# Kernel tuning notes

Measured on AMD Instinct MI355X. Metric: run time of the kernel, lower is better.

Reference implementation:

```python
import jax, jax.numpy as jnp
import numpy as np

NUM_LYR = 4
HIDDEN = 64
IN_DIM = 3
EMBED = 64  # embed_dim // pnt_cond_steps


def setup_inputs() -> dict:
    key = jax.random.key(0)
    ks = jax.random.split(key, 10)
    s = 0.05
    return {
        "x": jax.random.normal(ks[0], (256, 1, 4096, IN_DIM), dtype=jnp.float32),
        "proj_in_w": jax.random.normal(ks[1], (HIDDEN, IN_DIM), dtype=jnp.float32) * s,
        "proj_in_b": jax.random.normal(ks[2], (HIDDEN,), dtype=jnp.float32) * s,
        "lyr_w": jax.random.normal(ks[3], (NUM_LYR, HIDDEN, HIDDEN), dtype=jnp.float32) * s,
        "lyr_b": jax.random.normal(ks[4], (NUM_LYR, HIDDEN), dtype=jnp.float32) * s,
        "glyr_w": jax.random.normal(ks[5], (NUM_LYR, HIDDEN, 2 * HIDDEN), dtype=jnp.float32) * s,
        "glyr_b": jax.random.normal(ks[6], (NUM_LYR, HIDDEN), dtype=jnp.float32) * s,
        "proj_out_w": jax.random.normal(ks[7], (EMBED, HIDDEN * NUM_LYR), dtype=jnp.float32) * s,
        "proj_out_b": jax.random.normal(ks[8], (EMBED,), dtype=jnp.float32) * s,
    }


def reference(x, proj_in_w, proj_in_b, lyr_w, lyr_b, glyr_w, glyr_b, proj_out_w, proj_out_b):
    b, t, l, d = x.shape  # t == pnt_cond_steps, l == num_point (no resampling)
    h = x.reshape(b * t, l, d)
    # proj_in + ReLU: [B, L, hidden]
    h = jax.nn.relu(jnp.einsum('bld,hd->blh', h, proj_in_w) + proj_in_b)
    xs = []
    for i in range(NUM_LYR):
        h = jax.nn.relu(jnp.einsum('blh,oh->blo', h, lyr_w[i]) + lyr_b[i])
        g = jnp.max(h, axis=1, keepdims=True)  # global max-pool over points
        gx = jnp.concatenate([h, jnp.broadcast_to(g, h.shape)], axis=2)  # [B, L, 2*hidden]
        h = jax.nn.relu(jnp.einsum('blc,oc->blo', gx, glyr_w[i]) + glyr_b[i])
        xs.append(h)
    feat = jnp.concatenate(xs, axis=2)  # [B, L, hidden*num_lyr]
    out = jnp.einsum('blc,ec->ble', feat, proj_out_w) + proj_out_b
    out = jnp.max(out, axis=1)  # [B, embed]
    # rearrange '(b t) d -> b (d t)'
    out = out.reshape(b, t, -1)
    out = jnp.transpose(out, (0, 2, 1)).reshape(b, -1)
    return out
```

## Files before the change

### kernel.cpp

```cpp
#include <hip/hip_runtime.h>

#define HH   64
#define BPTS 256
#define LPB  4096
#define NBAT 256
#define NPTS (NBAT * LPB)

typedef _Float16 f16x8 __attribute__((ext_vector_type(8)));
typedef float    f32x4 __attribute__((ext_vector_type(4)));

__device__ __forceinline__ int fofs(int r, int c) {
    return (r << 6) | ((((c >> 3) ^ (r & 7))) << 3) | (c & 7);
}
__device__ __forceinline__ int bofs(int r, int m) {
    return (r << 6) | ((m ^ (r & 7)) << 3);
}
__device__ __forceinline__ f16x8 rd8(const _Float16* p, int r, int m) {
    return *(const f16x8*)&p[bofs(r, m)];
}

__device__ __forceinline__ void split2(float v, _Float16& h, _Float16& l) {
    h = (_Float16)v;
    l = (_Float16)(v - (float)h);
}

__device__ __forceinline__ void mfma_gemm(const _Float16* ah_, const _Float16* al_,
                                          const _Float16* wh_, const _Float16* wl_,
                                          int rb, int lane, f32x4 acc[2][4]) {
    const int rA = rb + (lane & 15);
    const int cB = lane & 15;
    const int g  = lane >> 4;
#pragma unroll
    for (int s = 0; s < 2; ++s) {
        const int m = s * 4 + g;
        f16x8 Ah[2], Al[2];
#pragma unroll
        for (int rt = 0; rt < 2; ++rt) {
            Ah[rt] = rd8(ah_, rA + 16 * rt, m);
            Al[rt] = rd8(al_, rA + 16 * rt, m);
        }
#pragma unroll
        for (int ct = 0; ct < 4; ++ct) {
            f16x8 Bh = rd8(wh_, cB + 16 * ct, m);
            f16x8 Bl = rd8(wl_, cB + 16 * ct, m);
#pragma unroll
            for (int rt = 0; rt < 2; ++rt) {
                acc[rt][ct] = __builtin_amdgcn_mfma_f32_16x16x32_f16(Ah[rt], Bh, acc[rt][ct], 0, 0, 0);
                acc[rt][ct] = __builtin_amdgcn_mfma_f32_16x16x32_f16(Ah[rt], Bl, acc[rt][ct], 0, 0, 0);
                acc[rt][ct] = __builtin_amdgcn_mfma_f32_16x16x32_f16(Al[rt], Bh, acc[rt][ct], 0, 0, 0);
            }
        }
    }
}

__device__ __forceinline__ void write_acts(_Float16* hi, _Float16* lo,
                                           const f32x4 t[2][4], int rb, int lane) {
    const int g = lane >> 4, cb = lane & 15;
#pragma unroll
    for (int rt = 0; rt < 2; ++rt)
#pragma unroll
        for (int reg = 0; reg < 4; ++reg) {
            const int r = rb + 16 * rt + 4 * g + reg;
#pragma unroll
            for (int ct = 0; ct < 4; ++ct) {
                _Float16 h, l;
                split2(t[rt][ct][reg], h, l);
                const int o = fofs(r, 16 * ct + cb);
                hi[o] = h; lo[o] = l;
            }
        }
}

__device__ __forceinline__ void stage_w(_Float16* wh, _Float16* wl,
                                        const float* __restrict__ W, int tid, int ldw) {
    const int o = tid >> 3, k0 = (tid & 7) << 3;
    const float* wr = &W[(size_t)o * ldw + k0];
    float4 a = *(const float4*)wr;
    float4 b = *(const float4*)(wr + 4);
    float v[8] = {a.x, a.y, a.z, a.w, b.x, b.y, b.z, b.w};
    f16x8 h, l;
#pragma unroll
    for (int i = 0; i < 8; ++i) { _Float16 hh, ll; split2(v[i], hh, ll); h[i] = hh; l[i] = ll; }
    const int ofs = bofs(o, k0 >> 3);
    *(f16x8*)&wh[ofs] = h;
    *(f16x8*)&wl[ofs] = l;
}

__device__ __forceinline__ unsigned encf(float f) {
    unsigned u = __float_as_uint(f);
    return (u & 0x80000000u) ? ~u : (u | 0x80000000u);
}
__device__ __forceinline__ float decf(unsigned u) {
    return (u & 0x80000000u) ? __uint_as_float(u ^ 0x80000000u) : __uint_as_float(~u);
}

__global__ __launch_bounds__(256) void k_init(float* gbuf, unsigned* oenc) {
    int i = blockIdx.x * 256 + threadIdx.x;
    if (i < 4 * NBAT * HH) gbuf[i] = 0.0f;
    if (i < NBAT * HH)     oenc[i] = 0x007FFFFFu;
}

__global__ __launch_bounds__(64) void k_goff(const float* __restrict__ g,
                                             const float* __restrict__ gw,
                                             const float* __restrict__ gb,
                                             float* __restrict__ goff, int li) {
    const int b = blockIdx.x, o = threadIdx.x;
    const float* gr = &g[b * HH];
    const float* wr = &gw[(size_t)li * 64 * 128 + o * 128 + 64];
    float s = gb[li * 64 + o];
#pragma unroll
    for (int k = 0; k < 64; k += 4) {
        float4 w4 = *(const float4*)&wr[k];
        float4 g4 = *(const float4*)&gr[k];
        s = fmaf(g4.x, w4.x, fmaf(g4.y, w4.y, fmaf(g4.z, w4.z, fmaf(g4.w, w4.w, s))));
    }
    goff[(size_t)b * HH + o] = s;
}

template<int NSTAGE, bool DO_OUT>
__global__ __launch_bounds__(512, 4) void k_fused(
    const float* __restrict__ x, const float* __restrict__ piw,
    const float* __restrict__ pib, const float* __restrict__ lyrw,
    const float* __restrict__ lyrb, const float* __restrict__ gw,
    const float* __restrict__ pw, const float* __restrict__ pob,
    const float* __restrict__ goffb, float* __restrict__ gmax,
    unsigned* __restrict__ oenc) {
    __shared__ __align__(16) _Float16 a_hi[BPTS * HH];
    __shared__ __align__(16) _Float16 a_lo[BPTS * HH];
    __shared__ __align__(16) _Float16 w_hi[HH * HH];
    __shared__ __align__(16) _Float16 w_lo[HH * HH];
    const int tid  = threadIdx.x;
    const int lane = tid & 63, wave = tid >> 6;
    const int rb   = wave << 5;
    const int pbase = blockIdx.x * BPTS;
    const int b = pbase / LPB;
    int ch4[4];
#pragma unroll
    for (int ct = 0; ct < 4; ++ct) ch4[ct] = 16 * ct + (lane & 15);

    stage_w(w_hi, w_lo, lyrw, tid, 64);
    {
        const int p = tid >> 1, half = tid & 1;
        const size_t pidx = (size_t)(pbase + p) * 3;
        const float x0 = x[pidx], x1 = x[pidx + 1], x2 = x[pidx + 2];
#pragma unroll
        for (int j = 0; j < 4; ++j) {
            const int o0 = half * 32 + j * 8;
            f16x8 h, l;
#pragma unroll
            for (int i = 0; i < 8; ++i) {
                const int o = o0 + i;
                float v = fmaxf(fmaf(piw[o * 3], x0,
                              fmaf(piw[o * 3 + 1], x1,
                              fmaf(piw[o * 3 + 2], x2, pib[o]))), 0.0f);
                _Float16 hh, ll; split2(v, hh, ll);
                h[i] = hh; l[i] = ll;
            }
            const int ofs = bofs(p, o0 >> 3);
            *(f16x8*)&a_hi[ofs] = h;
            *(f16x8*)&a_lo[ofs] = l;
        }
    }
    __syncthreads();

    f32x4 acc[2][4];
#pragma unroll
    for (int rt = 0; rt < 2; ++rt)
#pragma unroll
        for (int ct = 0; ct < 4; ++ct) {
            const float bb = lyrb[ch4[ct]];
            acc[rt][ct] = (f32x4){bb, bb, bb, bb};
        }
    mfma_gemm(a_hi, a_lo, w_hi, w_lo, rb, lane, acc);

    f32x4 oacc[2][4];
    if (DO_OUT) {
#pragma unroll
        for (int rt = 0; rt < 2; ++rt)
#pragma unroll
            for (int ct = 0; ct < 4; ++ct) oacc[rt][ct] = (f32x4){0.f, 0.f, 0.f, 0.f};
    }

    constexpr int NITER = DO_OUT ? 4 : (NSTAGE - 1);
#pragma unroll
    for (int li = 0; li < NITER; ++li) {
#pragma unroll
        for (int rt = 0; rt < 2; ++rt)
#pragma unroll
            for (int ct = 0; ct < 4; ++ct)
#pragma unroll
                for (int r = 0; r < 4; ++r)
                    acc[rt][ct][r] = fmaxf(acc[rt][ct][r], 0.0f);

        __syncthreads();
        write_acts(a_hi, a_lo, acc, rb, lane);
        stage_w(w_hi, w_lo, &gw[(size_t)li * 64 * 128], tid, 128);
        __syncthreads();

        f32x4 a2[2][4];
#pragma unroll
        for (int rt = 0; rt < 2; ++rt)
#pragma unroll
            for (int ct = 0; ct < 4; ++ct) {
                const float gv = goffb[(size_t)li * NBAT * HH + (size_t)b * HH + ch4[ct]];
                a2[rt][ct] = (f32x4){gv, gv, gv, gv};
            }
        mfma_gemm(a_hi, a_lo, w_hi, w_lo, rb, lane, a2);
#pragma unroll
        for (int rt = 0; rt < 2; ++rt)
#pragma unroll
            for (int ct = 0; ct < 4; ++ct)
#pragma unroll
                for (int r = 0; r < 4; ++r)
                    a2[rt][ct][r] = fmaxf(a2[rt][ct][r], 0.0f);

        __syncthreads();
        write_acts(a_hi, a_lo, a2, rb, lane);
        if (DO_OUT) {
            stage_w(w_hi, w_lo, &pw[(size_t)li * 64], tid, 256);
            __syncthreads();
            mfma_gemm(a_hi, a_lo, w_hi, w_lo, rb, lane, oacc);
            if (li < 3) {
                __syncthreads();
                stage_w(w_hi, w_lo, &lyrw[(size_t)(li + 1) * 4096], tid, 64);
                __syncthreads();
            }
        } else {
            stage_w(w_hi, w_lo, &lyrw[(size_t)(li + 1) * 4096], tid, 64);
            __syncthreads();
        }
        if (li < 3) {
#pragma unroll
            for (int rt = 0; rt < 2; ++rt)
#pragma unroll
                for (int ct = 0; ct < 4; ++ct) {
                    const float bb = lyrb[(li + 1) * 64 + ch4[ct]];
                    acc[rt][ct] = (f32x4){bb, bb, bb, bb};
                }
            mfma_gemm(a_hi, a_lo, w_hi, w_lo, rb, lane, acc);
        }
    }

    float m4[4];
    if (!DO_OUT) {
#pragma unroll
        for (int ct = 0; ct < 4; ++ct) m4[ct] = 0.0f;
#pragma unroll
        for (int rt = 0; rt < 2; ++rt)
#pragma unroll
            for (int ct = 0; ct < 4; ++ct)
#pragma unroll
                for (int r = 0; r < 4; ++r)
                    m4[ct] = fmaxf(m4[ct], fmaxf(acc[rt][ct][r], 0.0f));
    } else {
#pragma unroll
        for (int ct = 0; ct < 4; ++ct) m4[ct] = -3.4e38f;
#pragma unroll
        for (int rt = 0; rt < 2; ++rt)
#pragma unroll
            for (int ct = 0; ct < 4; ++ct)
#pragma unroll
                for (int r = 0; r < 4; ++r)
                    m4[ct] = fmaxf(m4[ct], oacc[rt][ct][r]);
    }
#pragma unroll
    for (int ct = 0; ct < 4; ++ct) {
        m4[ct] = fmaxf(m4[ct], __shfl_xor(m4[ct], 16, 64));
        m4[ct] = fmaxf(m4[ct], __shfl_xor(m4[ct], 32, 64));
    }
    __syncthreads();
    float* red = (float*)a_hi;
    if ((lane >> 4) == 0)
#pragma unroll
        for (int ct = 0; ct < 4; ++ct)
            red[wave * 64 + ct * 16 + (lane & 15)] = m4[ct];
    __syncthreads();
    if (tid < 64) {
        float v = red[tid];
#pragma unroll
        for (int w = 1; w < 8; ++w) v = fmaxf(v, red[w * 64 + tid]);
        if (!DO_OUT)
            atomicMax((unsigned*)&gmax[b * HH + tid], __float_as_uint(v));
        else
            atomicMax(&oenc[b * HH + tid], encf(v + pob[tid]));
    }
}

__global__ __launch_bounds__(256) void k_dec(const unsigned* __restrict__ oenc,
                                             float* __restrict__ out) {
    int i = blockIdx.x * 256 + threadIdx.x;
    out[i] = decf(oenc[i]);
}

extern "C" void kernel_launch(void* const* d_in, const int* in_sizes, int n_in,
                              void* d_out, int out_size, void* d_ws, size_t ws_size,
                              hipStream_t stream) {
    const float* x    = (const float*)d_in[0];
    const float* piw  = (const float*)d_in[1];
    const float* pib  = (const float*)d_in[2];
    const float* lyrw = (const float*)d_in[3];
    const float* lyrb = (const float*)d_in[4];
    const float* gw   = (const float*)d_in[5];
    const float* gb   = (const float*)d_in[6];
    const float* pw   = (const float*)d_in[7];
    const float* pob  = (const float*)d_in[8];
    float* out = (float*)d_out;

    float* gbuf    = (float*)d_ws;
    unsigned* oenc = (unsigned*)(gbuf + 4 * NBAT * HH);
    float* goffbuf = (float*)(oenc + NBAT * HH);

    const int nblk = NPTS / BPTS;

    k_init<<<256, 256, 0, stream>>>(gbuf, oenc);

    k_fused<1, false><<<nblk, 512, 0, stream>>>(x, piw, pib, lyrw, lyrb, gw, pw, pob,
                                                goffbuf, gbuf, oenc);
    k_goff<<<NBAT, 64, 0, stream>>>(gbuf, gw, gb, goffbuf, 0);

    k_fused<2, false><<<nblk, 512, 0, stream>>>(x, piw, pib, lyrw, lyrb, gw, pw, pob,
                                                goffbuf, gbuf + NBAT * HH, oenc);
    k_goff<<<NBAT, 64, 0, stream>>>(gbuf + NBAT * HH, gw, gb, goffbuf + NBAT * HH, 1);

    k_fused<3, false><<<nblk, 512, 0, stream>>>(x, piw, pib, lyrw, lyrb, gw, pw, pob,
                                                goffbuf, gbuf + 2 * NBAT * HH, oenc);
    k_goff<<<NBAT, 64, 0, stream>>>(gbuf + 2 * NBAT * HH, gw, gb, goffbuf + 2 * NBAT * HH, 2);

    k_fused<4, false><<<nblk, 512, 0, stream>>>(x, piw, pib, lyrw, lyrb, gw, pw, pob,
                                                goffbuf, gbuf + 3 * NBAT * HH, oenc);
    k_goff<<<NBAT, 64, 0, stream>>>(gbuf + 3 * NBAT * HH, gw, gb, goffbuf + 3 * NBAT * HH, 3);

    k_fused<4, true><<<nblk, 512, 0, stream>>>(x, piw, pib, lyrw, lyrb, gw, pw, pob,
                                               goffbuf, nullptr, oenc);

    k_dec<<<(NBAT * HH) / 256, 256, 0, stream>>>(oenc, out);
}
```

Measured before the change: 1.058 ms.

## Materialize intermediate activations in workspace instead of recomputing prefix layers

The old code re-ran every earlier layer from the raw input in each of five passes, so the total compute grew quadratically with depth. The new code stores each layer's activations in global workspace as packed hi/lo fp16 pairs. It also keeps a running fp32 partial sum of the output projection, so each pass runs only one new layer. The small global-offset kernel is folded into the main kernels, each computing the offset per lane. This trades recomputation for large global memory traffic (about 268MB per activation buffer), and it depends on the workspace being large enough, with fallbacks for smaller sizes.

```diff
diff --git a/kernel.cpp b/kernel.cpp
--- a/kernel.cpp
+++ b/kernel.cpp
@@ -9,11 +9,13 @@
 typedef _Float16 f16x8 __attribute__((ext_vector_type(8)));
 typedef float    f32x4 __attribute__((ext_vector_type(4)));
 
+union HL { unsigned u; _Float16 f[2]; };
+
+__device__ __forceinline__ int bofs(int r, int m) {
+    return (r << 6) | ((m ^ (r & 7)) << 3);
+}
 __device__ __forceinline__ int fofs(int r, int c) {
     return (r << 6) | ((((c >> 3) ^ (r & 7))) << 3) | (c & 7);
-}
-__device__ __forceinline__ int bofs(int r, int m) {
-    return (r << 6) | ((m ^ (r & 7)) << 3);
 }
 __device__ __forceinline__ f16x8 rd8(const _Float16* p, int r, int m) {
     return *(const f16x8*)&p[bofs(r, m)];
@@ -22,6 +24,9 @@
 __device__ __forceinline__ void split2(float v, _Float16& h, _Float16& l) {
     h = (_Float16)v;
     l = (_Float16)(v - (float)h);
+}
+__device__ __forceinline__ unsigned pack_hilo(float v) {
+    HL u; split2(v, u.f[0], u.f[1]); return u.u;
 }
 
 __device__ __forceinline__ void mfma_gemm(const _Float16* ah_, const _Float16* al_,
@@ -86,6 +91,41 @@
     *(f16x8*)&wl[ofs] = l;
 }
 
+__device__ __forceinline__ void stage_u(_Float16* hi, _Float16* lo,
+                                        const unsigned* __restrict__ u,
+                                        int pbase, int tid) {
+    const int row = tid >> 1, c0 = (tid & 1) << 5;
+    const unsigned* src = &u[(size_t)(pbase + row) * HH + c0];
+#pragma unroll
+    for (int j = 0; j < 4; ++j) {
+        uint4 qa = *(const uint4*)&src[j * 8];
+        uint4 qb = *(const uint4*)&src[j * 8 + 4];
+        unsigned q[8] = {qa.x, qa.y, qa.z, qa.w, qb.x, qb.y, qb.z, qb.w};
+        f16x8 h, l;
+#pragma unroll
+        for (int i = 0; i < 8; ++i) { HL v; v.u = q[i]; h[i] = v.f[0]; l[i] = v.f[1]; }
+        const int ofs = bofs(row, (c0 >> 3) + j);
+        *(f16x8*)&hi[ofs] = h;
+        *(f16x8*)&lo[ofs] = l;
+    }
+}
+
+__device__ __forceinline__ float goff_lane_calc(const float* __restrict__ gall,
+                                                const float* __restrict__ gw,
+                                                const float* __restrict__ gb,
+                                                int li, int b, int lane) {
+    const float* gr = &gall[((size_t)li * NBAT + b) * HH];
+    const float* wr = &gw[((size_t)li * 64 + lane) * 128 + 64];
+    float s = gb[li * 64 + lane];
+#pragma unroll
+    for (int k = 0; k < 64; k += 4) {
+        float4 w4 = *(const float4*)&wr[k];
+        float4 g4 = *(const float4*)&gr[k];
+        s = fmaf(g4.x, w4.x, fmaf(g4.y, w4.y, fmaf(g4.z, w4.z, fmaf(g4.w, w4.w, s))));
+    }
+    return s;
+}
+
 __device__ __forceinline__ unsigned encf(float f) {
     unsigned u = __float_as_uint(f);
     return (u & 0x80000000u) ? ~u : (u | 0x80000000u);
@@ -100,38 +140,278 @@
     if (i < NBAT * HH)     oenc[i] = 0x007FFFFFu;
 }
 
-__global__ __launch_bounds__(64) void k_goff(const float* __restrict__ g,
-                                             const float* __restrict__ gw,
-                                             const float* __restrict__ gb,
-                                             float* __restrict__ goff, int li) {
-    const int b = blockIdx.x, o = threadIdx.x;
-    const float* gr = &g[b * HH];
-    const float* wr = &gw[(size_t)li * 64 * 128 + o * 128 + 64];
-    float s = gb[li * 64 + o];
-#pragma unroll
-    for (int k = 0; k < 64; k += 4) {
-        float4 w4 = *(const float4*)&wr[k];
-        float4 g4 = *(const float4*)&gr[k];
-        s = fmaf(g4.x, w4.x, fmaf(g4.y, w4.y, fmaf(g4.z, w4.z, fmaf(g4.w, w4.w, s))));
-    }
-    goff[(size_t)b * HH + o] = s;
-}
+#define PROJ_IN_PROLOGUE()                                                      \
+    {                                                                           \
+        const int p = tid >> 1, half = tid & 1;                                 \
+        const size_t pidx = (size_t)(pbase + p) * 3;                            \
+        const float x0 = x[pidx], x1 = x[pidx + 1], x2 = x[pidx + 2];           \
+        for (int j = 0; j < 4; ++j) {                                           \
+            const int o0 = half * 32 + j * 8;                                   \
+            f16x8 h, l;                                                         \
+            for (int i = 0; i < 8; ++i) {                                       \
+                const int o = o0 + i;                                           \
+                float v = fmaxf(fmaf(piw[o * 3], x0,                            \
+                              fmaf(piw[o * 3 + 1], x1,                          \
+                              fmaf(piw[o * 3 + 2], x2, pib[o]))), 0.0f);        \
+                _Float16 hh, ll; split2(v, hh, ll);                             \
+                h[i] = hh; l[i] = ll;                                           \
+            }                                                                   \
+            const int ofs = bofs(p, o0 >> 3);                                   \
+            *(f16x8*)&a_hi[ofs] = h;                                            \
+            *(f16x8*)&a_lo[ofs] = l;                                            \
+        }                                                                       \
+    }
+
+#define MAX_EPILOGUE(ATOMIC_STMT)                                               \
+    {                                                                           \
+        for (int ct = 0; ct < 4; ++ct) {                                        \
+            m4[ct] = fmaxf(m4[ct], __shfl_xor(m4[ct], 16, 64));                 \
+            m4[ct] = fmaxf(m4[ct], __shfl_xor(m4[ct], 32, 64));                 \
+        }                                                                       \
+        __syncthreads();                                                        \
+        float* red = (float*)a_hi;                                              \
+        if ((lane >> 4) == 0)                                                   \
+            for (int ct = 0; ct < 4; ++ct)                                      \
+                red[wave * 64 + ct * 16 + (lane & 15)] = m4[ct];                \
+        __syncthreads();                                                        \
+        if (tid < 64) {                                                         \
+            float v = red[tid];                                                 \
+            for (int w = 1; w < 8; ++w) v = fmaxf(v, red[w * 64 + tid]);        \
+            ATOMIC_STMT;                                                        \
+        }                                                                       \
+    }
+
+
+__global__ __launch_bounds__(512, 4) void k_p0s(
+    const float* __restrict__ x, const float* __restrict__ piw,
+    const float* __restrict__ pib, const float* __restrict__ lyrw,
+    const float* __restrict__ lyrb, unsigned* __restrict__ u,
+    float* __restrict__ gout) {
+    __shared__ __align__(16) _Float16 a_hi[BPTS * HH];
+    __shared__ __align__(16) _Float16 a_lo[BPTS * HH];
+    __shared__ __align__(16) _Float16 w_hi[HH * HH];
+    __shared__ __align__(16) _Float16 w_lo[HH * HH];
+    const int tid = threadIdx.x, lane = tid & 63, wave = tid >> 6;
+    const int rb = wave << 5;
+    const int pbase = blockIdx.x * BPTS;
+    const int b = pbase / LPB;
+    int ch4[4];
+#pragma unroll
+    for (int ct = 0; ct < 4; ++ct) ch4[ct] = 16 * ct + (lane & 15);
+
+    stage_w(w_hi, w_lo, lyrw, tid, 64);
+    PROJ_IN_PROLOGUE();
+    __syncthreads();
+
+    f32x4 acc[2][4];
+#pragma unroll
+    for (int rt = 0; rt < 2; ++rt)
+#pragma unroll
+        for (int ct = 0; ct < 4; ++ct) {
+            const float bb = lyrb[ch4[ct]];
+            acc[rt][ct] = (f32x4){bb, bb, bb, bb};
+        }
+    mfma_gemm(a_hi, a_lo, w_hi, w_lo, rb, lane, acc);
+
+    const int g = lane >> 4;
+    float m4[4] = {0.f, 0.f, 0.f, 0.f};
+#pragma unroll
+    for (int rt = 0; rt < 2; ++rt)
+#pragma unroll
+        for (int reg = 0; reg < 4; ++reg) {
+            const int r = rb + 16 * rt + 4 * g + reg;
+            unsigned* dst = &u[(size_t)(pbase + r) * HH];
+#pragma unroll
+            for (int ct = 0; ct < 4; ++ct) {
+                float v = fmaxf(acc[rt][ct][reg], 0.0f);
+                m4[ct] = fmaxf(m4[ct], v);
+                dst[ch4[ct]] = pack_hilo(v);
+            }
+        }
+    MAX_EPILOGUE(atomicMax((unsigned*)&gout[b * HH + tid], __float_as_uint(v)));
+}
+
+template<bool DO_POUT>
+__global__ __launch_bounds__(512, 4) void k_midS(
+    unsigned* __restrict__ u, float* __restrict__ partial,
+    const float* __restrict__ gall, float* __restrict__ gout,
+    const float* __restrict__ gw, const float* __restrict__ gb,
+    const float* __restrict__ lyrw, const float* __restrict__ lyrb,
+    const float* __restrict__ pw, int li, int accflag) {
+    __shared__ __align__(16) _Float16 a_hi[BPTS * HH];
+    __shared__ __align__(16) _Float16 a_lo[BPTS * HH];
+    __shared__ __align__(16) _Float16 w_hi[HH * HH];
+    __shared__ __align__(16) _Float16 w_lo[HH * HH];
+    const int tid = threadIdx.x, lane = tid & 63, wave = tid >> 6;
+    const int rb = wave << 5;
+    const int pbase = blockIdx.x * BPTS;
+    const int b = pbase / LPB;
+    const int g = lane >> 4;
+    int ch4[4];
+#pragma unroll
+    for (int ct = 0; ct < 4; ++ct) ch4[ct] = 16 * ct + (lane & 15);
+
+    stage_u(a_hi, a_lo, u, pbase, tid);
+    stage_w(w_hi, w_lo, &gw[(size_t)li * 64 * 128], tid, 128);
+    const float gl = goff_lane_calc(gall, gw, gb, li, b, lane);
+    __syncthreads();
+
+    f32x4 a2[2][4];
+#pragma unroll
+    for (int ct = 0; ct < 4; ++ct) {
+        const float gv = __shfl(gl, ch4[ct], 64);
+#pragma unroll
+        for (int rt = 0; rt < 2; ++rt) a2[rt][ct] = (f32x4){gv, gv, gv, gv};
+    }
+    mfma_gemm(a_hi, a_lo, w_hi, w_lo, rb, lane, a2);
+#pragma unroll
+    for (int rt = 0; rt < 2; ++rt)
+#pragma unroll
+        for (int ct = 0; ct < 4; ++ct)
+#pragma unroll
+            for (int r = 0; r < 4; ++r)
+                a2[rt][ct][r] = fmaxf(a2[rt][ct][r], 0.0f);
+    __syncthreads();
+
+    write_acts(a_hi, a_lo, a2, rb, lane);
+    if (DO_POUT) {
+        stage_w(w_hi, w_lo, &pw[(size_t)li * 64], tid, 256);
+        __syncthreads();
+        f32x4 oacc[2][4];
+#pragma unroll
+        for (int rt = 0; rt < 2; ++rt)
+#pragma unroll
+            for (int ct = 0; ct < 4; ++ct) oacc[rt][ct] = (f32x4){0.f, 0.f, 0.f, 0.f};
+        mfma_gemm(a_hi, a_lo, w_hi, w_lo, rb, lane, oacc);
+#pragma unroll
+        for (int rt = 0; rt < 2; ++rt)
+#pragma unroll
+            for (int reg = 0; reg < 4; ++reg) {
+                const int r = rb + 16 * rt + 4 * g + reg;
+                float* pr = &partial[(size_t)(pbase + r) * HH];
+#pragma unroll
+                for (int ct = 0; ct < 4; ++ct) {
+                    float v = oacc[rt][ct][reg];
+                    if (accflag) v += pr[ch4[ct]];
+                    pr[ch4[ct]] = v;
+                }
+            }
+        __syncthreads();
+        stage_w(w_hi, w_lo, &lyrw[(size_t)(li + 1) * 4096], tid, 64);
+        __syncthreads();
+    } else {
+        stage_w(w_hi, w_lo, &lyrw[(size_t)(li + 1) * 4096], tid, 64);
+        __syncthreads();
+    }
+
+    f32x4 acc[2][4];
+#pragma unroll
+    for (int rt = 0; rt < 2; ++rt)
+#pragma unroll
+        for (int ct = 0; ct < 4; ++ct) {
+            const float bb = lyrb[(li + 1) * 64 + ch4[ct]];
+            acc[rt][ct] = (f32x4){bb, bb, bb, bb};
+        }
+    mfma_gemm(a_hi, a_lo, w_hi, w_lo, rb, lane, acc);
+
+    float m4[4] = {0.f, 0.f, 0.f, 0.f};
+#pragma unroll
+    for (int rt = 0; rt < 2; ++rt)
+#pragma unroll
+        for (int reg = 0; reg < 4; ++reg) {
+            const int r = rb + 16 * rt + 4 * g + reg;
+            unsigned* dst = &u[(size_t)(pbase + r) * HH];
+#pragma unroll
+            for (int ct = 0; ct < 4; ++ct) {
+                float v = fmaxf(acc[rt][ct][reg], 0.0f);
+                m4[ct] = fmaxf(m4[ct], v);
+                dst[ch4[ct]] = pack_hilo(v);
+            }
+        }
+    MAX_EPILOGUE(atomicMax((unsigned*)&gout[b * HH + tid], __float_as_uint(v)));
+}
+
+__global__ __launch_bounds__(512, 4) void k_lastS(
+    const unsigned* __restrict__ u, const float* __restrict__ partial,
+    const float* __restrict__ gall, const float* __restrict__ gw,
+    const float* __restrict__ gb, const float* __restrict__ pw,
+    const float* __restrict__ pob, unsigned* __restrict__ oenc) {
+    __shared__ __align__(16) _Float16 a_hi[BPTS * HH];
+    __shared__ __align__(16) _Float16 a_lo[BPTS * HH];
+    __shared__ __align__(16) _Float16 w_hi[HH * HH];
+    __shared__ __align__(16) _Float16 w_lo[HH * HH];
+    const int tid = threadIdx.x, lane = tid & 63, wave = tid >> 6;
+    const int rb = wave << 5;
+    const int pbase = blockIdx.x * BPTS;
+    const int b = pbase / LPB;
+    const int g = lane >> 4;
+    const int li = 3;
+    int ch4[4];
+#pragma unroll
+    for (int ct = 0; ct < 4; ++ct) ch4[ct] = 16 * ct + (lane & 15);
+
+    stage_u(a_hi, a_lo, u, pbase, tid);
+    stage_w(w_hi, w_lo, &gw[(size_t)li * 64 * 128], tid, 128);
+    const float gl = goff_lane_calc(gall, gw, gb, li, b, lane);
+    __syncthreads();
+
+    f32x4 a2[2][4];
+#pragma unroll
+    for (int ct = 0; ct < 4; ++ct) {
+        const float gv = __shfl(gl, ch4[ct], 64);
+#pragma unroll
+        for (int rt = 0; rt < 2; ++rt) a2[rt][ct] = (f32x4){gv, gv, gv, gv};
+    }
+    mfma_gemm(a_hi, a_lo, w_hi, w_lo, rb, lane, a2);
+#pragma unroll
+    for (int rt = 0; rt < 2; ++rt)
+#pragma unroll
+        for (int ct = 0; ct < 4; ++ct)
+#pragma unroll
+            for (int r = 0; r < 4; ++r)
+                a2[rt][ct][r] = fmaxf(a2[rt][ct][r], 0.0f);
+    __syncthreads();
+
+    write_acts(a_hi, a_lo, a2, rb, lane);
+    stage_w(w_hi, w_lo, &pw[(size_t)li * 64], tid, 256);
+    __syncthreads();
+
+    f32x4 oacc[2][4];
+#pragma unroll
+    for (int rt = 0; rt < 2; ++rt)
+#pragma unroll
+        for (int ct = 0; ct < 4; ++ct) oacc[rt][ct] = (f32x4){0.f, 0.f, 0.f, 0.f};
+    mfma_gemm(a_hi, a_lo, w_hi, w_lo, rb, lane, oacc);
+
+    float m4[4] = {-3.4e38f, -3.4e38f, -3.4e38f, -3.4e38f};
+#pragma unroll
+    for (int rt = 0; rt < 2; ++rt)
+#pragma unroll
+        for (int reg = 0; reg < 4; ++reg) {
+            const int r = rb + 16 * rt + 4 * g + reg;
+            const float* pr = &partial[(size_t)(pbase + r) * HH];
+#pragma unroll
+            for (int ct = 0; ct < 4; ++ct)
+                m4[ct] = fmaxf(m4[ct], oacc[rt][ct][reg] + pr[ch4[ct]]);
+        }
+    MAX_EPILOGUE(atomicMax(&oenc[b * HH + tid], encf(v + pob[tid])));
+}
+
 
 template<int NSTAGE, bool DO_OUT>
 __global__ __launch_bounds__(512, 4) void k_fused(
     const float* __restrict__ x, const float* __restrict__ piw,
     const float* __restrict__ pib, const float* __restrict__ lyrw,
     const float* __restrict__ lyrb, const float* __restrict__ gw,
-    const float* __restrict__ pw, const float* __restrict__ pob,
-    const float* __restrict__ goffb, float* __restrict__ gmax,
-    unsigned* __restrict__ oenc) {
+    const float* __restrict__ gb, const float* __restrict__ pw,
+    const float* __restrict__ pob, const float* __restrict__ gall,
+    float* __restrict__ gmax, unsigned* __restrict__ oenc) {
     __shared__ __align__(16) _Float16 a_hi[BPTS * HH];
     __shared__ __align__(16) _Float16 a_lo[BPTS * HH];
     __shared__ __align__(16) _Float16 w_hi[HH * HH];
     __shared__ __align__(16) _Float16 w_lo[HH * HH];
-    const int tid  = threadIdx.x;
-    const int lane = tid & 63, wave = tid >> 6;
-    const int rb   = wave << 5;
+    const int tid = threadIdx.x, lane = tid & 63, wave = tid >> 6;
+    const int rb = wave << 5;
     const int pbase = blockIdx.x * BPTS;
     const int b = pbase / LPB;
     int ch4[4];
@@ -139,28 +419,7 @@
     for (int ct = 0; ct < 4; ++ct) ch4[ct] = 16 * ct + (lane & 15);
 
     stage_w(w_hi, w_lo, lyrw, tid, 64);
-    {
-        const int p = tid >> 1, half = tid & 1;
-        const size_t pidx = (size_t)(pbase + p) * 3;
-        const float x0 = x[pidx], x1 = x[pidx + 1], x2 = x[pidx + 2];
-#pragma unroll
-        for (int j = 0; j < 4; ++j) {
-            const int o0 = half * 32 + j * 8;
-            f16x8 h, l;
-#pragma unroll
-            for (int i = 0; i < 8; ++i) {
-                const int o = o0 + i;
-                float v = fmaxf(fmaf(piw[o * 3], x0,
-                              fmaf(piw[o * 3 + 1], x1,
-                              fmaf(piw[o * 3 + 2], x2, pib[o]))), 0.0f);
-                _Float16 hh, ll; split2(v, hh, ll);
-                h[i] = hh; l[i] = ll;
-            }
-            const int ofs = bofs(p, o0 >> 3);
-            *(f16x8*)&a_hi[ofs] = h;
-            *(f16x8*)&a_lo[ofs] = l;
-        }
-    }
+    PROJ_IN_PROLOGUE();
     __syncthreads();
 
     f32x4 acc[2][4];
@@ -195,16 +454,16 @@
         __syncthreads();
         write_acts(a_hi, a_lo, acc, rb, lane);
         stage_w(w_hi, w_lo, &gw[(size_t)li * 64 * 128], tid, 128);
+        const float gl = goff_lane_calc(gall, gw, gb, li, b, lane);
         __syncthreads();
 
         f32x4 a2[2][4];
 #pragma unroll
-        for (int rt = 0; rt < 2; ++rt)
-#pragma unroll
-            for (int ct = 0; ct < 4; ++ct) {
-                const float gv = goffb[(size_t)li * NBAT * HH + (size_t)b * HH + ch4[ct]];
-                a2[rt][ct] = (f32x4){gv, gv, gv, gv};
-            }
+        for (int ct = 0; ct < 4; ++ct) {
+            const float gv = __shfl(gl, ch4[ct], 64);
+#pragma unroll
+            for (int rt = 0; rt < 2; ++rt) a2[rt][ct] = (f32x4){gv, gv, gv, gv};
+        }
         mfma_gemm(a_hi, a_lo, w_hi, w_lo, rb, lane, a2);
 #pragma unroll
         for (int rt = 0; rt < 2; ++rt)
@@ -252,6 +511,7 @@
 #pragma unroll
                 for (int r = 0; r < 4; ++r)
                     m4[ct] = fmaxf(m4[ct], fmaxf(acc[rt][ct][r], 0.0f));
+        MAX_EPILOGUE(atomicMax((unsigned*)&gmax[b * HH + tid], __float_as_uint(v)));
     } else {
 #pragma unroll
         for (int ct = 0; ct < 4; ++ct) m4[ct] = -3.4e38f;
@@ -262,27 +522,7 @@
 #pragma unroll
                 for (int r = 0; r < 4; ++r)
                     m4[ct] = fmaxf(m4[ct], oacc[rt][ct][r]);
-    }
-#pragma unroll
-    for (int ct = 0; ct < 4; ++ct) {
-        m4[ct] = fmaxf(m4[ct], __shfl_xor(m4[ct], 16, 64));
-        m4[ct] = fmaxf(m4[ct], __shfl_xor(m4[ct], 32, 64));
-    }
-    __syncthreads();
-    float* red = (float*)a_hi;
-    if ((lane >> 4) == 0)
-#pragma unroll
-        for (int ct = 0; ct < 4; ++ct)
-            red[wave * 64 + ct * 16 + (lane & 15)] = m4[ct];
-    __syncthreads();
-    if (tid < 64) {
-        float v = red[tid];
-#pragma unroll
-        for (int w = 1; w < 8; ++w) v = fmaxf(v, red[w * 64 + tid]);
-        if (!DO_OUT)
-            atomicMax((unsigned*)&gmax[b * HH + tid], __float_as_uint(v));
-        else
-            atomicMax(&oenc[b * HH + tid], encf(v + pob[tid]));
+        MAX_EPILOGUE(atomicMax(&oenc[b * HH + tid], encf(v + pob[tid])));
     }
 }
 
@@ -306,32 +546,60 @@
     const float* pob  = (const float*)d_in[8];
     float* out = (float*)d_out;
 
-    float* gbuf    = (float*)d_ws;
-    unsigned* oenc = (unsigned*)(gbuf + 4 * NBAT * HH);
-    float* goffbuf = (float*)(oenc + NBAT * HH);
-
     const int nblk = NPTS / BPTS;
-
-    k_init<<<256, 256, 0, stream>>>(gbuf, oenc);
-
-    k_fused<1, false><<<nblk, 512, 0, stream>>>(x, piw, pib, lyrw, lyrb, gw, pw, pob,
-                                                goffbuf, gbuf, oenc);
-    k_goff<<<NBAT, 64, 0, stream>>>(gbuf, gw, gb, goffbuf, 0);
-
-    k_fused<2, false><<<nblk, 512, 0, stream>>>(x, piw, pib, lyrw, lyrb, gw, pw, pob,
-                                                goffbuf, gbuf + NBAT * HH, oenc);
-    k_goff<<<NBAT, 64, 0, stream>>>(gbuf + NBAT * HH, gw, gb, goffbuf + NBAT * HH, 1);
-
-    k_fused<3, false><<<nblk, 512, 0, stream>>>(x, piw, pib, lyrw, lyrb, gw, pw, pob,
-                                                goffbuf, gbuf + 2 * NBAT * HH, oenc);
-    k_goff<<<NBAT, 64, 0, stream>>>(gbuf + 2 * NBAT * HH, gw, gb, goffbuf + 2 * NBAT * HH, 2);
-
-    k_fused<4, false><<<nblk, 512, 0, stream>>>(x, piw, pib, lyrw, lyrb, gw, pw, pob,
-                                                goffbuf, gbuf + 3 * NBAT * HH, oenc);
-    k_goff<<<NBAT, 64, 0, stream>>>(gbuf + 3 * NBAT * HH, gw, gb, goffbuf + 3 * NBAT * HH, 3);
-
-    k_fused<4, true><<<nblk, 512, 0, stream>>>(x, piw, pib, lyrw, lyrb, gw, pw, pob,
-                                               goffbuf, nullptr, oenc);
-
-    k_dec<<<(NBAT * HH) / 256, 256, 0, stream>>>(oenc, out);
-}
+    const size_t UB    = (size_t)NPTS * HH * 4;
+    const size_t PB    = (size_t)NPTS * HH * 4;
+    const size_t SMALL = (size_t)5 * NBAT * HH * 4;
+    const size_t NEED12 = UB + PB + SMALL;
+    const size_t NEED19 = UB + SMALL;
+
+    if (ws_size >= NEED12) {
+        unsigned* u    = (unsigned*)d_ws;
+        float* partial = (float*)(u + (size_t)NPTS * HH);
+        float* gbuf    = partial + (size_t)NPTS * HH;
+        unsigned* oenc = (unsigned*)(gbuf + 4 * NBAT * HH);
+
+        k_init<<<256, 256, 0, stream>>>(gbuf, oenc);
+        k_p0s<<<nblk, 512, 0, stream>>>(x, piw, pib, lyrw, lyrb, u, gbuf);
+        k_midS<true><<<nblk, 512, 0, stream>>>(u, partial, gbuf, gbuf + 1 * NBAT * HH,
+                                               gw, gb, lyrw, lyrb, pw, 0, 0);
+        k_midS<true><<<nblk, 512, 0, stream>>>(u, partial, gbuf, gbuf + 2 * NBAT * HH,
+                                               gw, gb, lyrw, lyrb, pw, 1, 1);
+        k_midS<true><<<nblk, 512, 0, stream>>>(u, partial, gbuf, gbuf + 3 * NBAT * HH,
+                                               gw, gb, lyrw, lyrb, pw, 2, 1);
+        k_lastS<<<nblk, 512, 0, stream>>>(u, partial, gbuf, gw, gb, pw, pob, oenc);
+        k_dec<<<(NBAT * HH) / 256, 256, 0, stream>>>(oenc, out);
+    } else if (ws_size >= NEED19) {
+        unsigned* u    = (unsigned*)d_ws;
+        float* gbuf    = (float*)(u + (size_t)NPTS * HH);
+        unsigned* oenc = (unsigned*)(gbuf + 4 * NBAT * HH);
+
+        k_init<<<256, 256, 0, stream>>>(gbuf, oenc);
+        k_p0s<<<nblk, 512, 0, stream>>>(x, piw, pib, lyrw, lyrb, u, gbuf);
+        k_midS<false><<<nblk, 512, 0, stream>>>(u, nullptr, gbuf, gbuf + 1 * NBAT * HH,
+                                                gw, gb, lyrw, lyrb, pw, 0, 0);
+        k_midS<false><<<nblk, 512, 0, stream>>>(u, nullptr, gbuf, gbuf + 2 * NBAT * HH,
+                                                gw, gb, lyrw, lyrb, pw, 1, 0);
+        k_midS<false><<<nblk, 512, 0, stream>>>(u, nullptr, gbuf, gbuf + 3 * NBAT * HH,
+                                                gw, gb, lyrw, lyrb, pw, 2, 0);
+        k_fused<4, true><<<nblk, 512, 0, stream>>>(x, piw, pib, lyrw, lyrb, gw, gb, pw, pob,
+                                                   gbuf, nullptr, oenc);
+        k_dec<<<(NBAT * HH) / 256, 256, 0, stream>>>(oenc, out);
+    } else {
+        float* gbuf    = (float*)d_ws;
+        unsigned* oenc = (unsigned*)(gbuf + 4 * NBAT * HH);
+
+        k_init<<<256, 256, 0, stream>>>(gbuf, oenc);
+        k_fused<1, false><<<nblk, 512, 0, stream>>>(x, piw, pib, lyrw, lyrb, gw, gb, pw, pob,
+                                                    gbuf, gbuf, oenc);
+        k_fused<2, false><<<nblk, 512, 0, stream>>>(x, piw, pib, lyrw, lyrb, gw, gb, pw, pob,
+                                                    gbuf, gbuf + 1 * NBAT * HH, oenc);
+        k_fused<3, false><<<nblk, 512, 0, stream>>>(x, piw, pib, lyrw, lyrb, gw, gb, pw, pob,
+                                                    gbuf, gbuf + 2 * NBAT * HH, oenc);
+        k_fused<4, false><<<nblk, 512, 0, stream>>>(x, piw, pib, lyrw, lyrb, gw, gb, pw, pob,
+                                                    gbuf, gbuf + 3 * NBAT * HH, oenc);
+        k_fused<4, true><<<nblk, 512, 0, stream>>>(x, piw, pib, lyrw, lyrb, gw, gb, pw, pob,
+                                                   gbuf, nullptr, oenc);
+        k_dec<<<(NBAT * HH) / 256, 256, 0, stream>>>(oenc, out);
+    }
+}
```

New measurement: 1.423 ms. 1.34x slower.

## Materialize per-stage activations in global memory instead of recomputing prefix layers

Applied to the files above, without the earlier changes.

Replaces the recompute-from-input scheme, where each pass reran every earlier layer up to the current global max-pool, with stage kernels that store the post-ReLU activations as packed fp16 hi/lo pairs. They also keep a running fp32 partial sum of the output projection in global buffers. Each stage reloads the stored activations, applies the global-conditioned layer, adds its projection contribution, and runs the next layer. This removes the repeated MFMA work of the earlier layers, which grows with stage depth. In exchange it adds large global traffic: about 256 MB of activations and 256 MB of partials per stage, with a read-modify-write of the partials.

```diff
diff --git a/kernel.cpp b/kernel.cpp
--- a/kernel.cpp
+++ b/kernel.cpp
@@ -9,11 +9,19 @@
 typedef _Float16 f16x8 __attribute__((ext_vector_type(8)));
 typedef float    f32x4 __attribute__((ext_vector_type(4)));
 
+union HL { unsigned u; _Float16 f[2]; };
+
+__device__ unsigned u_buf[(size_t)NPTS * HH];
+__device__ float    partial_buf[(size_t)NPTS * HH];
+__device__ float    g_buf[4 * NBAT * HH];
+__device__ float    goff_buf[4 * NBAT * HH];
+__device__ unsigned oenc_buf[NBAT * HH];
+
+__device__ __forceinline__ int bofs(int r, int m) {
+    return (r << 6) | ((m ^ (r & 7)) << 3);
+}
 __device__ __forceinline__ int fofs(int r, int c) {
     return (r << 6) | ((((c >> 3) ^ (r & 7))) << 3) | (c & 7);
-}
-__device__ __forceinline__ int bofs(int r, int m) {
-    return (r << 6) | ((m ^ (r & 7)) << 3);
 }
 __device__ __forceinline__ f16x8 rd8(const _Float16* p, int r, int m) {
     return *(const f16x8*)&p[bofs(r, m)];
@@ -22,6 +30,9 @@
 __device__ __forceinline__ void split2(float v, _Float16& h, _Float16& l) {
     h = (_Float16)v;
     l = (_Float16)(v - (float)h);
+}
+__device__ __forceinline__ unsigned pack_hilo(float v) {
+    HL u; split2(v, u.f[0], u.f[1]); return u.u;
 }
 
 __device__ __forceinline__ void mfma_gemm(const _Float16* ah_, const _Float16* al_,
@@ -86,6 +97,23 @@
     *(f16x8*)&wl[ofs] = l;
 }
 
+__device__ __forceinline__ void stage_u(_Float16* hi, _Float16* lo, int pbase, int tid) {
+    const int row = tid >> 1, c0 = (tid & 1) << 5;
+    const unsigned* src = &u_buf[(size_t)(pbase + row) * HH + c0];
+#pragma unroll
+    for (int j = 0; j < 4; ++j) {
+        uint4 qa = *(const uint4*)&src[j * 8];
+        uint4 qb = *(const uint4*)&src[j * 8 + 4];
+        unsigned q[8] = {qa.x, qa.y, qa.z, qa.w, qb.x, qb.y, qb.z, qb.w};
+        f16x8 h, l;
+#pragma unroll
+        for (int i = 0; i < 8; ++i) { HL v; v.u = q[i]; h[i] = v.f[0]; l[i] = v.f[1]; }
+        const int ofs = bofs(row, (c0 >> 3) + j);
+        *(f16x8*)&hi[ofs] = h;
+        *(f16x8*)&lo[ofs] = l;
+    }
+}
+
 __device__ __forceinline__ unsigned encf(float f) {
     unsigned u = __float_as_uint(f);
     return (u & 0x80000000u) ? ~u : (u | 0x80000000u);
@@ -94,19 +122,17 @@
     return (u & 0x80000000u) ? __uint_as_float(u ^ 0x80000000u) : __uint_as_float(~u);
 }
 
-__global__ __launch_bounds__(256) void k_init(float* gbuf, unsigned* oenc) {
+__global__ __launch_bounds__(256) void k_init() {
     int i = blockIdx.x * 256 + threadIdx.x;
-    if (i < 4 * NBAT * HH) gbuf[i] = 0.0f;
-    if (i < NBAT * HH)     oenc[i] = 0x007FFFFFu;
-}
-
-__global__ __launch_bounds__(64) void k_goff(const float* __restrict__ g,
-                                             const float* __restrict__ gw,
-                                             const float* __restrict__ gb,
-                                             float* __restrict__ goff, int li) {
+    if (i < 4 * NBAT * HH) g_buf[i] = 0.0f;
+    if (i < NBAT * HH)     oenc_buf[i] = 0x007FFFFFu;
+}
+
+__global__ __launch_bounds__(64) void k_goff(const float* __restrict__ gw,
+                                             const float* __restrict__ gb, int li) {
     const int b = blockIdx.x, o = threadIdx.x;
-    const float* gr = &g[b * HH];
-    const float* wr = &gw[(size_t)li * 64 * 128 + o * 128 + 64];
+    const float* gr = &g_buf[((size_t)li * NBAT + b) * HH];
+    const float* wr = &gw[((size_t)li * 64 + o) * 128 + 64];
     float s = gb[li * 64 + o];
 #pragma unroll
     for (int k = 0; k < 64; k += 4) {
@@ -114,24 +140,38 @@
         float4 g4 = *(const float4*)&gr[k];
         s = fmaf(g4.x, w4.x, fmaf(g4.y, w4.y, fmaf(g4.z, w4.z, fmaf(g4.w, w4.w, s))));
     }
-    goff[(size_t)b * HH + o] = s;
-}
-
-template<int NSTAGE, bool DO_OUT>
-__global__ __launch_bounds__(512, 4) void k_fused(
+    goff_buf[((size_t)li * NBAT + b) * HH + o] = s;
+}
+
+#define MAX_EPILOGUE(ATOMIC_STMT)                                               \
+    {                                                                           \
+        for (int ct = 0; ct < 4; ++ct) {                                        \
+            m4[ct] = fmaxf(m4[ct], __shfl_xor(m4[ct], 16, 64));                 \
+            m4[ct] = fmaxf(m4[ct], __shfl_xor(m4[ct], 32, 64));                 \
+        }                                                                       \
+        __syncthreads();                                                        \
+        float* red = (float*)a_hi;                                              \
+        if ((lane >> 4) == 0)                                                   \
+            for (int ct = 0; ct < 4; ++ct)                                      \
+                red[wave * 64 + ct * 16 + (lane & 15)] = m4[ct];                \
+        __syncthreads();                                                        \
+        if (tid < 64) {                                                         \
+            float v = red[tid];                                                 \
+            for (int w = 1; w < 8; ++w) v = fmaxf(v, red[w * 64 + tid]);        \
+            ATOMIC_STMT;                                                        \
+        }                                                                       \
+    }
+
+__global__ __launch_bounds__(512, 4) void k_p0s(
     const float* __restrict__ x, const float* __restrict__ piw,
     const float* __restrict__ pib, const float* __restrict__ lyrw,
-    const float* __restrict__ lyrb, const float* __restrict__ gw,
-    const float* __restrict__ pw, const float* __restrict__ pob,
-    const float* __restrict__ goffb, float* __restrict__ gmax,
-    unsigned* __restrict__ oenc) {
+    const float* __restrict__ lyrb) {
     __shared__ __align__(16) _Float16 a_hi[BPTS * HH];
     __shared__ __align__(16) _Float16 a_lo[BPTS * HH];
     __shared__ __align__(16) _Float16 w_hi[HH * HH];
     __shared__ __align__(16) _Float16 w_lo[HH * HH];
-    const int tid  = threadIdx.x;
-    const int lane = tid & 63, wave = tid >> 6;
-    const int rb   = wave << 5;
+    const int tid = threadIdx.x, lane = tid & 63, wave = tid >> 6;
+    const int rb = wave << 5;
     const int pbase = blockIdx.x * BPTS;
     const int b = pbase / LPB;
     int ch4[4];
@@ -173,123 +213,183 @@
         }
     mfma_gemm(a_hi, a_lo, w_hi, w_lo, rb, lane, acc);
 
+    const int g = lane >> 4;
+    float m4[4] = {0.f, 0.f, 0.f, 0.f};
+#pragma unroll
+    for (int rt = 0; rt < 2; ++rt)
+#pragma unroll
+        for (int reg = 0; reg < 4; ++reg) {
+            const int r = rb + 16 * rt + 4 * g + reg;
+            unsigned* dst = &u_buf[(size_t)(pbase + r) * HH];
+#pragma unroll
+            for (int ct = 0; ct < 4; ++ct) {
+                float v = fmaxf(acc[rt][ct][reg], 0.0f);
+                m4[ct] = fmaxf(m4[ct], v);
+                dst[ch4[ct]] = pack_hilo(v);
+            }
+        }
+    MAX_EPILOGUE(atomicMax((unsigned*)&g_buf[b * HH + tid], __float_as_uint(v)));
+}
+
+__global__ __launch_bounds__(512, 4) void k_midS(
+    const float* __restrict__ gw, const float* __restrict__ lyrw,
+    const float* __restrict__ lyrb, const float* __restrict__ pw,
+    int li, int accflag) {
+    __shared__ __align__(16) _Float16 a_hi[BPTS * HH];
+    __shared__ __align__(16) _Float16 a_lo[BPTS * HH];
+    __shared__ __align__(16) _Float16 w_hi[HH * HH];
+    __shared__ __align__(16) _Float16 w_lo[HH * HH];
+    const int tid = threadIdx.x, lane = tid & 63, wave = tid >> 6;
+    const int rb = wave << 5;
+    const int pbase = blockIdx.x * BPTS;
+    const int b = pbase / LPB;
+    const int g = lane >> 4;
+    int ch4[4];
+#pragma unroll
+    for (int ct = 0; ct < 4; ++ct) ch4[ct] = 16 * ct + (lane & 15);
+
+    stage_u(a_hi, a_lo, pbase, tid);
+    stage_w(w_hi, w_lo, &gw[(size_t)li * 64 * 128], tid, 128);
+    __syncthreads();
+
+    f32x4 a2[2][4];
+#pragma unroll
+    for (int ct = 0; ct < 4; ++ct) {
+        const float gv = goff_buf[((size_t)li * NBAT + b) * HH + ch4[ct]];
+#pragma unroll
+        for (int rt = 0; rt < 2; ++rt) a2[rt][ct] = (f32x4){gv, gv, gv, gv};
+    }
+    mfma_gemm(a_hi, a_lo, w_hi, w_lo, rb, lane, a2);
+#pragma unroll
+    for (int rt = 0; rt < 2; ++rt)
+#pragma unroll
+        for (int ct = 0; ct < 4; ++ct)
+#pragma unroll
+            for (int r = 0; r < 4; ++r)
+                a2[rt][ct][r] = fmaxf(a2[rt][ct][r], 0.0f);
+    __syncthreads();
+
+    write_acts(a_hi, a_lo, a2, rb, lane);
+    stage_w(w_hi, w_lo, &pw[(size_t)li * 64], tid, 256);
+    __syncthreads();
+
     f32x4 oacc[2][4];
-    if (DO_OUT) {
-#pragma unroll
-        for (int rt = 0; rt < 2; ++rt)
-#pragma unroll
-            for (int ct = 0; ct < 4; ++ct) oacc[rt][ct] = (f32x4){0.f, 0.f, 0.f, 0.f};
-    }
-
-    constexpr int NITER = DO_OUT ? 4 : (NSTAGE - 1);
-#pragma unroll
-    for (int li = 0; li < NITER; ++li) {
-#pragma unroll
-        for (int rt = 0; rt < 2; ++rt)
+#pragma unroll
+    for (int rt = 0; rt < 2; ++rt)
+#pragma unroll
+        for (int ct = 0; ct < 4; ++ct) oacc[rt][ct] = (f32x4){0.f, 0.f, 0.f, 0.f};
+    mfma_gemm(a_hi, a_lo, w_hi, w_lo, rb, lane, oacc);
+#pragma unroll
+    for (int rt = 0; rt < 2; ++rt)
+#pragma unroll
+        for (int reg = 0; reg < 4; ++reg) {
+            const int r = rb + 16 * rt + 4 * g + reg;
+            float* pr = &partial_buf[(size_t)(pbase + r) * HH];
+#pragma unroll
+            for (int ct = 0; ct < 4; ++ct) {
+                float v = oacc[rt][ct][reg];
+                if (accflag) v += pr[ch4[ct]];
+                pr[ch4[ct]] = v;
+            }
+        }
+    __syncthreads();
+    stage_w(w_hi, w_lo, &lyrw[(size_t)(li + 1) * 4096], tid, 64);
+    __syncthreads();
+
+    f32x4 acc[2][4];
+#pragma unroll
+    for (int rt = 0; rt < 2; ++rt)
+#pragma unroll
+        for (int ct = 0; ct < 4; ++ct) {
+            const float bb = lyrb[(li + 1) * 64 + ch4[ct]];
+            acc[rt][ct] = (f32x4){bb, bb, bb, bb};
+        }
+    mfma_gemm(a_hi, a_lo, w_hi, w_lo, rb, lane, acc);
+
+    float m4[4] = {0.f, 0.f, 0.f, 0.f};
+#pragma unroll
+    for (int rt = 0; rt < 2; ++rt)
+#pragma unroll
+        for (int reg = 0; reg < 4; ++reg) {
+            const int r = rb + 16 * rt + 4 * g + reg;
+            unsigned* dst = &u_buf[(size_t)(pbase + r) * HH];
+#pragma unroll
+            for (int ct = 0; ct < 4; ++ct) {
+                float v = fmaxf(acc[rt][ct][reg], 0.0f);
+                m4[ct] = fmaxf(m4[ct], v);
+                dst[ch4[ct]] = pack_hilo(v);
+            }
+        }
+    MAX_EPILOGUE(atomicMax((unsigned*)&g_buf[((size_t)(li + 1) * NBAT + b) * HH + tid],
+                           __float_as_uint(v)));
+}
+
+__global__ __launch_bounds__(512, 4) void k_lastS(
+    const float* __restrict__ gw, const float* __restrict__ pw,
+    const float* __restrict__ pob) {
+    __shared__ __align__(16) _Float16 a_hi[BPTS * HH];
+    __shared__ __align__(16) _Float16 a_lo[BPTS * HH];
+    __shared__ __align__(16) _Float16 w_hi[HH * HH];
+    __shared__ __align__(16) _Float16 w_lo[HH * HH];
+    const int tid = threadIdx.x, lane = tid & 63, wave = tid >> 6;
+    const int rb = wave << 5;
+    const int pbase = blockIdx.x * BPTS;
+    const int b = pbase / LPB;
+    const int g = lane >> 4;
+    const int li = 3;
+    int ch4[4];
+#pragma unroll
+    for (int ct = 0; ct < 4; ++ct) ch4[ct] = 16 * ct + (lane & 15);
+
+    stage_u(a_hi, a_lo, pbase, tid);
+    stage_w(w_hi, w_lo, &gw[(size_t)li * 64 * 128], tid, 128);
+    __syncthreads();
+
+    f32x4 a2[2][4];
+#pragma unroll
+    for (int ct = 0; ct < 4; ++ct) {
+        const float gv = goff_buf[((size_t)li * NBAT + b) * HH + ch4[ct]];
+#pragma unroll
+        for (int rt = 0; rt < 2; ++rt) a2[rt][ct] = (f32x4){gv, gv, gv, gv};
+    }
+    mfma_gemm(a_hi, a_lo, w_hi, w_lo, rb, lane, a2);
+#pragma unroll
+    for (int rt = 0; rt < 2; ++rt)
+#pragma unroll
+        for (int ct = 0; ct < 4; ++ct)
+#pragma unroll
+            for (int r = 0; r < 4; ++r)
+                a2[rt][ct][r] = fmaxf(a2[rt][ct][r], 0.0f);
+    __syncthreads();
+
+    write_acts(a_hi, a_lo, a2, rb, lane);
+    stage_w(w_hi, w_lo, &pw[(size_t)li * 64], tid, 256);
+    __syncthreads();
+
+    f32x4 oacc[2][4];
+#pragma unroll
+    for (int rt = 0; rt < 2; ++rt)
+#pragma unroll
+        for (int ct = 0; ct < 4; ++ct) oacc[rt][ct] = (f32x4){0.f, 0.f, 0.f, 0.f};
+    mfma_gemm(a_hi, a_lo, w_hi, w_lo, rb, lane, oacc);
+
+    float m4[4] = {-3.4e38f, -3.4e38f, -3.4e38f, -3.4e38f};
+#pragma unroll
+    for (int rt = 0; rt < 2; ++rt)
+#pragma unroll
+        for (int reg = 0; reg < 4; ++reg) {
+            const int r = rb + 16 * rt + 4 * g + reg;
+            const float* pr = &partial_buf[(size_t)(pbase + r) * HH];
 #pragma unroll
             for (int ct = 0; ct < 4; ++ct)
-#pragma unroll
-                for (int r = 0; r < 4; ++r)
-                    acc[rt][ct][r] = fmaxf(acc[rt][ct][r], 0.0f);
-
-        __syncthreads();
-        write_acts(a_hi, a_lo, acc, rb, lane);
-        stage_w(w_hi, w_lo, &gw[(size_t)li * 64 * 128], tid, 128);
-        __syncthreads();
-
-        f32x4 a2[2][4];
-#pragma unroll
-        for (int rt = 0; rt < 2; ++rt)
-#pragma unroll
-            for (int ct = 0; ct < 4; ++ct) {
-                const float gv = goffb[(size_t)li * NBAT * HH + (size_t)b * HH + ch4[ct]];
-                a2[rt][ct] = (f32x4){gv, gv, gv, gv};
-            }
-        mfma_gemm(a_hi, a_lo, w_hi, w_lo, rb, lane, a2);
-#pragma unroll
-        for (int rt = 0; rt < 2; ++rt)
-#pragma unroll
-            for (int ct = 0; ct < 4; ++ct)
-#pragma unroll
-                for (int r = 0; r < 4; ++r)
-                    a2[rt][ct][r] = fmaxf(a2[rt][ct][r], 0.0f);
-
-        __syncthreads();
-        write_acts(a_hi, a_lo, a2, rb, lane);
-        if (DO_OUT) {
-            stage_w(w_hi, w_lo, &pw[(size_t)li * 64], tid, 256);
-            __syncthreads();
-            mfma_gemm(a_hi, a_lo, w_hi, w_lo, rb, lane, oacc);
-            if (li < 3) {
-                __syncthreads();
-                stage_w(w_hi, w_lo, &lyrw[(size_t)(li + 1) * 4096], tid, 64);
-                __syncthreads();
-            }
-        } else {
-            stage_w(w_hi, w_lo, &lyrw[(size_t)(li + 1) * 4096], tid, 64);
-            __syncthreads();
-        }
-        if (li < 3) {
-#pragma unroll
-            for (int rt = 0; rt < 2; ++rt)
-#pragma unroll
-                for (int ct = 0; ct < 4; ++ct) {
-                    const float bb = lyrb[(li + 1) * 64 + ch4[ct]];
-                    acc[rt][ct] = (f32x4){bb, bb, bb, bb};
-                }
-            mfma_gemm(a_hi, a_lo, w_hi, w_lo, rb, lane, acc);
-        }
-    }
-
-    float m4[4];
-    if (!DO_OUT) {
-#pragma unroll
-        for (int ct = 0; ct < 4; ++ct) m4[ct] = 0.0f;
-#pragma unroll
-        for (int rt = 0; rt < 2; ++rt)
-#pragma unroll
-            for (int ct = 0; ct < 4; ++ct)
-#pragma unroll
-                for (int r = 0; r < 4; ++r)
-                    m4[ct] = fmaxf(m4[ct], fmaxf(acc[rt][ct][r], 0.0f));
-    } else {
-#pragma unroll
-        for (int ct = 0; ct < 4; ++ct) m4[ct] = -3.4e38f;
-#pragma unroll
-        for (int rt = 0; rt < 2; ++rt)
-#pragma unroll
-            for (int ct = 0; ct < 4; ++ct)
-#pragma unroll
-                for (int r = 0; r < 4; ++r)
-                    m4[ct] = fmaxf(m4[ct], oacc[rt][ct][r]);
-    }
-#pragma unroll
-    for (int ct = 0; ct < 4; ++ct) {
-        m4[ct] = fmaxf(m4[ct], __shfl_xor(m4[ct], 16, 64));
-        m4[ct] = fmaxf(m4[ct], __shfl_xor(m4[ct], 32, 64));
-    }
-    __syncthreads();
-    float* red = (float*)a_hi;
-    if ((lane >> 4) == 0)
-#pragma unroll
-        for (int ct = 0; ct < 4; ++ct)
-            red[wave * 64 + ct * 16 + (lane & 15)] = m4[ct];
-    __syncthreads();
-    if (tid < 64) {
-        float v = red[tid];
-#pragma unroll
-        for (int w = 1; w < 8; ++w) v = fmaxf(v, red[w * 64 + tid]);
-        if (!DO_OUT)
-            atomicMax((unsigned*)&gmax[b * HH + tid], __float_as_uint(v));
-        else
-            atomicMax(&oenc[b * HH + tid], encf(v + pob[tid]));
-    }
-}
-
-__global__ __launch_bounds__(256) void k_dec(const unsigned* __restrict__ oenc,
-                                             float* __restrict__ out) {
+                m4[ct] = fmaxf(m4[ct], oacc[rt][ct][reg] + pr[ch4[ct]]);
+        }
+    MAX_EPILOGUE(atomicMax(&oenc_buf[b * HH + tid], encf(v + pob[tid])));
+}
+
+__global__ __launch_bounds__(256) void k_dec(float* __restrict__ out) {
     int i = blockIdx.x * 256 + threadIdx.x;
-    out[i] = decf(oenc[i]);
+    out[i] = decf(oenc_buf[i]);
 }
 
 extern "C" void kernel_launch(void* const* d_in, const int* in_sizes, int n_in,
@@ -306,32 +406,22 @@
     const float* pob  = (const float*)d_in[8];
     float* out = (float*)d_out;
 
-    float* gbuf    = (float*)d_ws;
-    unsigned* oenc = (unsigned*)(gbuf + 4 * NBAT * HH);
-    float* goffbuf = (float*)(oenc + NBAT * HH);
-
     const int nblk = NPTS / BPTS;
 
-    k_init<<<256, 256, 0, stream>>>(gbuf, oenc);
-
-    k_fused<1, false><<<nblk, 512, 0, stream>>>(x, piw, pib, lyrw, lyrb, gw, pw, pob,
-                                                goffbuf, gbuf, oenc);
-    k_goff<<<NBAT, 64, 0, stream>>>(gbuf, gw, gb, goffbuf, 0);
-
-    k_fused<2, false><<<nblk, 512, 0, stream>>>(x, piw, pib, lyrw, lyrb, gw, pw, pob,
-                                                goffbuf, gbuf + NBAT * HH, oenc);
-    k_goff<<<NBAT, 64, 0, stream>>>(gbuf + NBAT * HH, gw, gb, goffbuf + NBAT * HH, 1);
-
-    k_fused<3, false><<<nblk, 512, 0, stream>>>(x, piw, pib, lyrw, lyrb, gw, pw, pob,
-                                                goffbuf, gbuf + 2 * NBAT * HH, oenc);
-    k_goff<<<NBAT, 64, 0, stream>>>(gbuf + 2 * NBAT * HH, gw, gb, goffbuf + 2 * NBAT * HH, 2);
-
-    k_fused<4, false><<<nblk, 512, 0, stream>>>(x, piw, pib, lyrw, lyrb, gw, pw, pob,
-                                                goffbuf, gbuf + 3 * NBAT * HH, oenc);
-    k_goff<<<NBAT, 64, 0, stream>>>(gbuf + 3 * NBAT * HH, gw, gb, goffbuf + 3 * NBAT * HH, 3);
-
-    k_fused<4, true><<<nblk, 512, 0, stream>>>(x, piw, pib, lyrw, lyrb, gw, pw, pob,
-                                               goffbuf, nullptr, oenc);
-
-    k_dec<<<(NBAT * HH) / 256, 256, 0, stream>>>(oenc, out);
-}
+    k_init<<<256, 256, 0, stream>>>();
+    k_p0s<<<nblk, 512, 0, stream>>>(x, piw, pib, lyrw, lyrb);
+
+    k_goff<<<NBAT, 64, 0, stream>>>(gw, gb, 0);
+    k_midS<<<nblk, 512, 0, stream>>>(gw, lyrw, lyrb, pw, 0, 0);
+
+    k_goff<<<NBAT, 64, 0, stream>>>(gw, gb, 1);
+    k_midS<<<nblk, 512, 0, stream>>>(gw, lyrw, lyrb, pw, 1, 1);
+
+    k_goff<<<NBAT, 64, 0, stream>>>(gw, gb, 2);
+    k_midS<<<nblk, 512, 0, stream>>>(gw, lyrw, lyrb, pw, 2, 1);
+
+    k_goff<<<NBAT, 64, 0, stream>>>(gw, gb, 3);
+    k_lastS<<<nblk, 512, 0, stream>>>(gw, pw, pob);
+
+    k_dec<<<(NBAT * HH) / 256, 256, 0, stream>>>(out);
+}
```

Result: slower. 1.138 ms (+7.5%).
